# Optimization experiments

Measured on AMD Instinct MI355X. Metric: run time of the kernel, lower is better.

The kernel has to match this reference:

```python
import jax, jax.numpy as jnp
import numpy as np

B, T, D_MODEL = 4, 4096, 512
HEADS, BUCKET_SIZE, N_HASHES = 8, 64, 4
DIM_HEAD = D_MODEL // HEADS  # 64
D_FFN = 2048
N_BUCKETS = T // BUCKET_SIZE  # 64
SELF_ATTN_VALUE = -5e4  # reformer TOKEN_SELF_ATTN_VALUE


def setup_inputs() -> dict:
    key = jax.random.key(0)
    ks = jax.random.split(key, 16)
    s = 0.02
    return {
        'x': jax.random.normal(ks[0], (B, T, D_MODEL), jnp.float32),
        'rotations': jax.random.normal(ks[1], (DIM_HEAD, N_HASHES, N_BUCKETS // 2), jnp.float32),
        'w_qk': jax.random.normal(ks[2], (D_MODEL, D_MODEL), jnp.float32) * s,
        'w_v': jax.random.normal(ks[3], (D_MODEL, D_MODEL), jnp.float32) * s,
        'w_out': jax.random.normal(ks[4], (D_MODEL, D_MODEL), jnp.float32) * s,
        'b_out': jnp.zeros((D_MODEL,), jnp.float32),
        'ln1_g': jnp.ones((D_MODEL,), jnp.float32),
        'ln1_b': jnp.zeros((D_MODEL,), jnp.float32),
        'w1': jax.random.normal(ks[5], (D_FFN, D_MODEL), jnp.float32) * s,
        'b1': jnp.zeros((D_FFN,), jnp.float32),
        'w2': jax.random.normal(ks[6], (D_MODEL, D_FFN), jnp.float32) * s,
        'b2': jnp.zeros((D_MODEL,), jnp.float32),
        'ln2_g': jnp.ones((D_MODEL,), jnp.float32),
        'ln2_b': jnp.zeros((D_MODEL,), jnp.float32),
    }


def layer_norm(x, g, b, eps=1e-6):
    m = x.mean(-1, keepdims=True)
    v = ((x - m) ** 2).mean(-1, keepdims=True)
    return (x - m) / jnp.sqrt(v + eps) * g + b


def look_one_back(x):
    # concat each chunk with the previous chunk (wrap-around), along in-chunk axis
    prev = jnp.roll(x, 1, axis=1)
    return jnp.concatenate([x, prev], axis=2)


def lsh_attention(qk, v, rotations):
    # qk, v: (bh, t, d) with shared-QK; rotations: (d, n_hashes, n_buckets//2)
    bh, t, d = qk.shape
    # --- hash: random rotations, argmax over [R, -R] ---
    rot = jnp.einsum('btf,fhi->bhti', qk, rotations)
    rot = jnp.concatenate([rot, -rot], axis=-1)        # (bh, H, t, n_buckets)
    buckets = jnp.argmax(rot, axis=-1)                 # (bh, H, t)
    buckets = buckets + (jnp.arange(N_HASHES) * N_BUCKETS)[None, :, None]
    buckets = buckets.reshape(bh, N_HASHES * t)
    # --- sort by (bucket, position) ---
    ticker = jnp.arange(N_HASHES * t)
    buckets_and_t = t * buckets + (ticker % t)[None, :]
    sticker = jnp.argsort(buckets_and_t, axis=-1)      # stable sort
    undo_sort = jnp.argsort(sticker, axis=-1)
    st = sticker % t                                   # original positions, sorted order
    sqk = jnp.take_along_axis(qk, st[..., None], axis=1)
    sv = jnp.take_along_axis(v, st[..., None], axis=1)
    # --- chunk: n_hashes*n_buckets chunks of bucket_size tokens ---
    n_chunks = N_HASHES * N_BUCKETS
    bq_t = st.reshape(bh, n_chunks, -1)
    bqk = sqk.reshape(bh, n_chunks, -1, d)
    bv = sv.reshape(bh, n_chunks, -1, d)
    bk = bqk / jnp.clip(jnp.linalg.norm(bqk, axis=-1, keepdims=True), 1e-6, None)
    bk = look_one_back(bk)
    bv = look_one_back(bv)
    bkv_t = look_one_back(bq_t)
    # --- local attention within chunk (+ previous chunk) ---
    dots = jnp.einsum('bcid,bcjd->bcij', bqk, bk) * (DIM_HEAD ** -0.5)
    self_mask = bq_t[..., None] == bkv_t[..., None, :]
    dots = jnp.where(self_mask, SELF_ATTN_VALUE, dots)
    logits = jax.nn.logsumexp(dots, axis=-1, keepdims=True)
    probs = jnp.exp(dots - logits)
    bo = jnp.einsum('bcij,bcjd->bcid', probs, bv)
    # --- unsort and combine hash rounds by softmax over round logits ---
    so = bo.reshape(bh, N_HASHES * t, d)
    slogits = logits.reshape(bh, N_HASHES * t)
    o = jnp.take_along_axis(so, undo_sort[..., None], axis=1).reshape(bh, N_HASHES, t, d)
    lg = jnp.take_along_axis(slogits, undo_sort, axis=1).reshape(bh, N_HASHES, t, 1)
    w = jnp.exp(lg - jax.nn.logsumexp(lg, axis=1, keepdims=True))
    return (o * w).sum(axis=1)                         # (bh, t, d)


def reference(x, rotations, w_qk, w_v, w_out, b_out, ln1_g, ln1_b, w1, b1, w2, b2, ln2_g, ln2_b):
    b, t, _ = x.shape
    qk = x @ w_qk.T
    v = x @ w_v.T

    def split_heads(u):
        return u.reshape(b, t, HEADS, DIM_HEAD).transpose(0, 2, 1, 3).reshape(b * HEADS, t, DIM_HEAD)

    attn = lsh_attention(split_heads(qk), split_heads(v), rotations)
    attn = attn.reshape(b, HEADS, t, DIM_HEAD).transpose(0, 2, 1, 3).reshape(b, t, D_MODEL)
    attn = attn @ w_out.T + b_out
    # residual + LN (dropout is identity at inference)
    h = layer_norm(attn + x, ln1_g, ln1_b)
    # position-wise FFN with its own residual + LN
    f = jax.nn.relu(h @ w1.T + b1) @ w2.T + b2
    return layer_norm(f + h, ln2_g, ln2_b)
```

## Files before the change

kernel.cpp:

```cpp
#include <hip/hip_runtime.h>
#include <stdint.h>

typedef unsigned short u16;
typedef __attribute__((ext_vector_type(4))) int   i32x4;
typedef __attribute__((ext_vector_type(4))) float f32x4;

__device__ __forceinline__ u16 f2bf(float x){
  unsigned int u = __float_as_uint(x);
  u += 0x7FFFu + ((u >> 16) & 1u);
  return (u16)(u >> 16);
}
__device__ __forceinline__ float bf2f(u16 h){
  return __uint_as_float(((unsigned int)h) << 16);
}
__device__ __forceinline__ unsigned int cvtpk_bf16(float lo, float hi){
  unsigned int r;
  asm("v_cvt_pk_bf16_f32 %0, %1, %2" : "=v"(r) : "v"(lo), "v"(hi));
  return r;
}
__device__ __forceinline__ f32x4 mfma16(i32x4 a, i32x4 b, f32x4 c){
  asm("v_mfma_f32_16x16x32_bf16 %0, %1, %2, %0" : "+v"(c) : "v"(a), "v"(b));
  return c;
}
__device__ __forceinline__ f32x4 acc_fence(f32x4 c){
  asm volatile("s_nop 7\ns_nop 7" : "+v"(c));
  return c;
}
__device__ __forceinline__ void gl_lds16(const void* g, void* l){
  unsigned long long ga = (unsigned long long)g;
  unsigned int la = (unsigned int)(unsigned long long)l;
  __builtin_amdgcn_global_load_lds((const __attribute__((address_space(1))) void*)ga,
                                   (__attribute__((address_space(3))) void*)la, 16, 0, 0);
}
__device__ __forceinline__ int xcd_swz(int f, int n){
  int chunk = n >> 3;
  return (f & 7) * chunk + (f >> 3);
}
__device__ __forceinline__ unsigned int f2mono(float v){
  unsigned int u = __float_as_uint(v);
  return u ^ ((unsigned int)((int)u >> 31) | 0x80000000u);
}
__device__ __forceinline__ float mono2f(unsigned int mu){
  unsigned int u = (mu & 0x80000000u) ? (mu ^ 0x80000000u) : ~mu;
  return __uint_as_float(u);
}
__device__ __forceinline__ unsigned long long shfl_xor_u64(unsigned long long x, int m){
  int lo = __shfl_xor((int)(unsigned int)(x & 0xFFFFFFFFull), m);
  int hi = __shfl_xor((int)(unsigned int)(x >> 32), m);
  return ((unsigned long long)(unsigned int)hi << 32) | (unsigned int)lo;
}

__global__ __launch_bounds__(256) void k_split(const float* __restrict__ in, u16* __restrict__ hi, u16* __restrict__ lo, int n4){
  int i = blockIdx.x*256 + threadIdx.x;
  if (i >= n4) return;
  float4 v = ((const float4*)in)[i];
  ushort4 h, l;
  h.x=f2bf(v.x); l.x=f2bf(v.x - bf2f(h.x));
  h.y=f2bf(v.y); l.y=f2bf(v.y - bf2f(h.y));
  h.z=f2bf(v.z); l.z=f2bf(v.z - bf2f(h.z));
  h.w=f2bf(v.w); l.w=f2bf(v.w - bf2f(h.w));
  ((ushort4*)hi)[i]=h; ((ushort4*)lo)[i]=l;
}

__global__ __launch_bounds__(256) void k_wprep(
    const float* __restrict__ w_qk, const float* __restrict__ w_v,
    const float* __restrict__ w_out, const float* __restrict__ w1,
    const float* __restrict__ w2, const float* __restrict__ rot,
    u16* __restrict__ wqkh, u16* __restrict__ wqkl,
    u16* __restrict__ wvb, u16* __restrict__ wob,
    u16* __restrict__ w1b, u16* __restrict__ w2b,
    u16* __restrict__ rothi, u16* __restrict__ rotlo)
{
  const int bid = blockIdx.x;
  if (bid >= 2816){
    int i = (bid - 2816)*256 + threadIdx.x;
    int d = i & 63, n = i >> 6;
    float v = rot[d*128 + n];
    u16 h = f2bf(v);
    rothi[i] = h; rotlo[i] = f2bf(v - bf2f(h));
    return;
  }
  const int i = bid*256 + threadIdx.x;
  if (i < 65536){
    float4 v = ((const float4*)w_qk)[i];
    ushort4 h, l;
    h.x=f2bf(v.x); l.x=f2bf(v.x - bf2f(h.x));
    h.y=f2bf(v.y); l.y=f2bf(v.y - bf2f(h.y));
    h.z=f2bf(v.z); l.z=f2bf(v.z - bf2f(h.z));
    h.w=f2bf(v.w); l.w=f2bf(v.w - bf2f(h.w));
    ((ushort4*)wqkh)[i]=h; ((ushort4*)wqkl)[i]=l;
    return;
  }
  const float* src; u16* dst; int j;
  if (i < 131072){ src = w_v;  dst = wvb; j = i - 65536; }
  else if (i < 196608){ src = w_out; dst = wob; j = i - 131072; }
  else if (i < 458752){ src = w1;   dst = w1b; j = i - 196608; }
  else { src = w2; dst = w2b; j = i - 458752; }
  float4 v = ((const float4*)src)[j];
  ushort4 o; o.x=f2bf(v.x); o.y=f2bf(v.y); o.z=f2bf(v.z); o.w=f2bf(v.w);
  ((ushort4*)dst)[j] = o;
}

template<int MODE>
__global__ __launch_bounds__(256) void k_gemm(
    const u16* __restrict__ A0, const u16* __restrict__ B0,
    const float* __restrict__ bias,
    float* __restrict__ Cf, u16* __restrict__ Cb,
    int M, int N, int K)
{
  const int tid = threadIdx.x;
  const int l = tid & 63, w = tid >> 6;
  const int lr = l & 15, lg = l >> 4;
  int flat = blockIdx.y * gridDim.x + blockIdx.x;
  flat = xcd_swz(flat, gridDim.x * gridDim.y);
  const int m0 = (flat / gridDim.x) * 128, n0 = (flat % gridDim.x) * 128;
  const int mbase = (w >> 1) * 64, nbase = (w & 1) * 64;

  __shared__ __align__(16) u16 As[128*64];
  __shared__ __align__(16) u16 Bs[128*64];

  f32x4 zero = {0.f,0.f,0.f,0.f};
  f32x4 acc[4][4];
  #pragma unroll
  for (int i=0;i<4;i++)
    #pragma unroll
    for (int j=0;j<4;j++) acc[i][j] = zero;

  const int row_s = tid >> 3;
  const int c16   = tid & 7;

  for (int k0 = 0; k0 < K; k0 += 64){
    #pragma unroll
    for (int q=0;q<4;q++){
      int ra = q*32 + row_s;
      int cs = c16 ^ (ra & 7);
      gl_lds16(A0 + (size_t)(m0 + ra)*K + k0 + cs*8, (char*)As + q*4096 + tid*16);
      gl_lds16(B0 + (size_t)(n0 + ra)*K + k0 + cs*8, (char*)Bs + q*4096 + tid*16);
    }
    __syncthreads();
    #pragma unroll
    for (int kk=0; kk<64; kk+=32){
      i32x4 af[4], bfr[4];
      #pragma unroll
      for (int mf=0;mf<4;mf++){
        int row = mbase + mf*16 + lr;
        af[mf] = *(const i32x4*)((const char*)As + row*128 + (((kk*2) + (lg*16)) ^ ((row&7)<<4)));
      }
      #pragma unroll
      for (int nf=0;nf<4;nf++){
        int row = nbase + nf*16 + lr;
        bfr[nf] = *(const i32x4*)((const char*)Bs + row*128 + (((kk*2) + (lg*16)) ^ ((row&7)<<4)));
      }
      #pragma unroll
      for (int mf=0;mf<4;mf++)
        #pragma unroll
        for (int nf=0;nf<4;nf++)
          acc[mf][nf] = mfma16(af[mf], bfr[nf], acc[mf][nf]);
    }
    __syncthreads();
  }

  #pragma unroll
  for (int mf=0;mf<4;mf++){
    #pragma unroll
    for (int nf=0;nf<4;nf++){
      f32x4 v = acc_fence(acc[mf][nf]);
      #pragma unroll
      for (int r=0;r<4;r++){
        int m = m0 + mbase + mf*16 + lg*4 + r;
        int n = n0 + nbase + nf*16 + lr;
        float val = v[r];
        if (MODE == 1){
          val += bias[n];
          val = fmaxf(val, 0.f);
          Cb[(size_t)m*N + n] = f2bf(val);
        } else if (MODE == 4){
          val += bias[n];
          Cb[(size_t)m*N + n] = f2bf(val);
        } else {
          int b = m >> 12, t = m & 4095, h = n >> 6, d = n & 63;
          size_t idx = ((((size_t)(b*8 + h)) << 12) + t)*64 + d;
          Cb[idx] = f2bf(val);
        }
      }
    }
  }
}

__global__ __launch_bounds__(256) void k_gemmqk(
    const u16* __restrict__ Ah, const u16* __restrict__ Al,
    const u16* __restrict__ Bh, const u16* __restrict__ Bl,
    u16* __restrict__ qb, u16* __restrict__ qlo, u16* __restrict__ kn)
{
  const int K = 512;
  const int tid = threadIdx.x;
  const int l = tid & 63, w = tid >> 6;
  const int lr = l & 15, lg = l >> 4;
  int flat = blockIdx.y * gridDim.x + blockIdx.x;
  flat = xcd_swz(flat, gridDim.x * gridDim.y);
  const int m0 = (flat >> 2) * 128, n0 = (flat & 3) * 128;
  const int mbase = (w >> 1) * 64, nbase = (w & 1) * 64;

  __shared__ __align__(16) u16 AsH[128*64];
  __shared__ __align__(16) u16 AsL[128*64];
  __shared__ __align__(16) u16 BsH[128*64];
  __shared__ __align__(16) u16 BsL[128*64];

  f32x4 zero = {0.f,0.f,0.f,0.f};
  f32x4 acc[4][4];
  #pragma unroll
  for (int i=0;i<4;i++)
    #pragma unroll
    for (int j=0;j<4;j++) acc[i][j] = zero;

  const int row_s = tid >> 3;
  const int c16   = tid & 7;

  for (int k0 = 0; k0 < K; k0 += 64){
    #pragma unroll
    for (int q=0;q<4;q++){
      int ra = q*32 + row_s;
      int cs = c16 ^ (ra & 7);
      size_t ao = (size_t)(m0 + ra)*K + k0 + cs*8;
      size_t bo = (size_t)(n0 + ra)*K + k0 + cs*8;
      gl_lds16(Ah + ao, (char*)AsH + q*4096 + tid*16);
      gl_lds16(Al + ao, (char*)AsL + q*4096 + tid*16);
      gl_lds16(Bh + bo, (char*)BsH + q*4096 + tid*16);
      gl_lds16(Bl + bo, (char*)BsL + q*4096 + tid*16);
    }
    __syncthreads();
    #pragma unroll
    for (int kk=0; kk<64; kk+=32){
      i32x4 ah[4], al[4], bh2[4], bl2[4];
      #pragma unroll
      for (int mf=0;mf<4;mf++){
        int row = mbase + mf*16 + lr;
        int off = (((kk*2) + (lg*16)) ^ ((row&7)<<4));
        ah[mf] = *(const i32x4*)((const char*)AsH + row*128 + off);
        al[mf] = *(const i32x4*)((const char*)AsL + row*128 + off);
      }
      #pragma unroll
      for (int nf=0;nf<4;nf++){
        int row = nbase + nf*16 + lr;
        int off = (((kk*2) + (lg*16)) ^ ((row&7)<<4));
        bh2[nf] = *(const i32x4*)((const char*)BsH + row*128 + off);
        bl2[nf] = *(const i32x4*)((const char*)BsL + row*128 + off);
      }
      #pragma unroll
      for (int mf=0;mf<4;mf++)
        #pragma unroll
        for (int nf=0;nf<4;nf++){
          acc[mf][nf] = mfma16(ah[mf], bh2[nf], acc[mf][nf]);
          acc[mf][nf] = mfma16(al[mf], bh2[nf], acc[mf][nf]);
          acc[mf][nf] = mfma16(ah[mf], bl2[nf], acc[mf][nf]);
        }
    }
    __syncthreads();
  }

  const int hh = (n0 + nbase) >> 6;
  #pragma unroll
  for (int mf=0;mf<4;mf++){
    f32x4 v[4];
    #pragma unroll
    for (int nf=0;nf<4;nf++) v[nf] = acc_fence(acc[mf][nf]);
    #pragma unroll
    for (int r=0;r<4;r++){
      float ss = 0.f;
      #pragma unroll
      for (int nf=0;nf<4;nf++) ss += v[nf][r]*v[nf][r];
      ss += __shfl_xor(ss, 1); ss += __shfl_xor(ss, 2);
      ss += __shfl_xor(ss, 4); ss += __shfl_xor(ss, 8);
      float scale = 0.18033688f / fmaxf(sqrtf(ss), 1e-6f);
      int m = m0 + mbase + mf*16 + lg*4 + r;
      int b = m >> 12, t = m & 4095;
      size_t rowb = ((((size_t)(b*8 + hh)) << 12) + t) * 64;
      #pragma unroll
      for (int nf=0;nf<4;nf++){
        float val = v[nf][r];
        u16 hbf = f2bf(val);
        size_t idx = rowb + nf*16 + lr;
        qb [idx] = hbf;
        qlo[idx] = f2bf(val - bf2f(hbf));
        kn [idx] = f2bf(val * scale);
      }
    }
  }
}

__global__ __launch_bounds__(256) void k_hash2(
    const u16* __restrict__ qh, const u16* __restrict__ ql,
    const u16* __restrict__ rh, const u16* __restrict__ rl,
    int* __restrict__ bkt)
{
  const int tid = threadIdx.x;
  const int l = tid & 63, w = tid >> 6, lr = l & 15, lg = l >> 4;
  __shared__ __align__(16) u16 Rh[128*64];
  __shared__ __align__(16) u16 Rl[128*64];
  {
    const int row_s = tid >> 3, c8 = tid & 7;
    #pragma unroll
    for (int q = 0; q < 4; q++){
      int ra = q*32 + row_s;
      int cs = c8 ^ (ra & 7);
      gl_lds16(rh + ra*64 + cs*8, (char*)Rh + q*4096 + tid*16);
      gl_lds16(rl + ra*64 + cs*8, (char*)Rl + q*4096 + tid*16);
    }
  }
  const int blk = xcd_swz(blockIdx.x, gridDim.x);
  const int qrow = blk*64 + w*16 + lr;
  const size_t qoff = (size_t)qrow*64;
  i32x4 qhf[2], qlf[2];
  qhf[0] = *(const i32x4*)(qh + qoff + lg*8);
  qhf[1] = *(const i32x4*)(qh + qoff + 32 + lg*8);
  qlf[0] = *(const i32x4*)(ql + qoff + lg*8);
  qlf[1] = *(const i32x4*)(ql + qoff + 32 + lg*8);
  __syncthreads();

  f32x4 zero = {0.f,0.f,0.f,0.f};
  f32x4 acc[8];
  #pragma unroll
  for (int i=0;i<8;i++) acc[i] = zero;
  #pragma unroll
  for (int ks = 0; ks < 2; ks++){
    #pragma unroll
    for (int nf = 0; nf < 8; nf++){
      int row = nf*16 + lr;
      int off = (ks*64 + lg*16) ^ ((row & 7) << 4);
      i32x4 rhf = *(const i32x4*)((const char*)Rh + row*128 + off);
      i32x4 rlf = *(const i32x4*)((const char*)Rl + row*128 + off);
      acc[nf] = mfma16(rhf, qhf[ks], acc[nf]);
      acc[nf] = mfma16(rlf, qhf[ks], acc[nf]);
      acc[nf] = mfma16(rhf, qlf[ks], acc[nf]);
    }
  }

  const int bh = qrow >> 12, t = qrow & 4095;
  #pragma unroll
  for (int hh = 0; hh < 4; hh++){
    f32x4 v0 = acc_fence(acc[2*hh]);
    f32x4 v1 = acc_fence(acc[2*hh+1]);
    unsigned long long kmax = 0, kmin = 0;
    #pragma unroll
    for (int r = 0; r < 4; r++){
      int j0 = lg*4 + r, j1 = 16 + lg*4 + r;
      unsigned int mu0 = f2mono(v0[r]), mu1 = f2mono(v1[r]);
      unsigned long long a = ((unsigned long long)mu0 << 32) | (unsigned int)(31 - j0);
      unsigned long long b = ((unsigned long long)mu1 << 32) | (unsigned int)(31 - j1);
      if (a > kmax) kmax = a;
      if (b > kmax) kmax = b;
      unsigned long long c = ((unsigned long long)(~mu0) << 32) | (unsigned int)(31 - j0);
      unsigned long long d = ((unsigned long long)(~mu1) << 32) | (unsigned int)(31 - j1);
      if (c > kmin) kmin = c;
      if (d > kmin) kmin = d;
    }
    #pragma unroll
    for (int msk = 16; msk < 64; msk <<= 1){
      unsigned long long o1 = shfl_xor_u64(kmax, msk); if (o1 > kmax) kmax = o1;
      unsigned long long o2 = shfl_xor_u64(kmin, msk); if (o2 > kmin) kmin = o2;
    }
    if (lg == 0){
      float vmax = mono2f((unsigned int)(kmax >> 32));
      int jmax = 31 - (int)(kmax & 0xFFFFFFFFull);
      float vmin = mono2f(~(unsigned int)(kmin >> 32));
      int jmin = 31 - (int)(kmin & 0xFFFFFFFFull);
      int bucket = (vmax >= -vmin) ? jmax : 32 + jmin;
      bkt[((size_t)(bh*4 + hh) << 12) + t] = bucket;
    }
  }
}

__global__ __launch_bounds__(64) void k_sort(const int* __restrict__ buckets, int* __restrict__ st){
  const int grp = blockIdx.x;
  const int t = threadIdx.x;
  __shared__ int bkL[4096];
  __shared__ int hist[64][65];
  __shared__ int tot[64];
  const size_t gbase = ((size_t)grp) << 12;
  for (int i=0;i<64;i++)
    bkL[i*64 + t] = buckets[gbase + i*64 + t];
  #pragma unroll
  for (int b=0;b<64;b++) hist[t][b] = 0;
  __syncthreads();
  for (int i=0;i<64;i++){
    int b = bkL[t*64 + i];
    hist[t][b]++;
  }
  __syncthreads();
  { int run = 0;
    for (int tt=0; tt<64; tt++){ int v = hist[tt][t]; hist[tt][t] = run; run += v; }
    tot[t] = run; }
  __syncthreads();
  { int v = tot[t]; int incl = v;
    #pragma unroll
    for (int d=1; d<64; d<<=1){ int n = __shfl_up(incl, d, 64); if (t >= d) incl += n; }
    tot[t] = incl - v; }
  __syncthreads();
  const size_t obase = (((size_t)(grp>>2)) << 14) + ((size_t)(grp&3) << 12);
  for (int i=0;i<64;i++){
    int e = t*64 + i;
    int b = bkL[e];
    int dest = tot[b] + hist[t][b];
    hist[t][b]++;
    st[obase + dest] = e;
  }
}

__global__ __launch_bounds__(256, 5) void k_attn(
    const u16* __restrict__ qb, const u16* __restrict__ kn, const u16* __restrict__ vB,
    const int* __restrict__ st, float* __restrict__ lgt_out, u16* __restrict__ bo)
{
  int flat = blockIdx.y * gridDim.x + blockIdx.x;
  flat = xcd_swz(flat, gridDim.x * gridDim.y);
  const int c = flat & 255, bh = flat >> 8;
  const int rnd = c >> 6;
  const int cprev = (c + 255) & 255;
  const int tid = threadIdx.x;
  const int l = tid & 63, w = tid >> 6, lr = l & 15, lg = l >> 4;

  __shared__ __align__(16) u16 Ks[128*64];
  __shared__ __align__(16) u16 Vt[64*128];

  const size_t stbase = ((size_t)bh) << 14;
  const size_t kvbase = ((size_t)bh) << 12;

  {
    const int rsub = l >> 3, c8 = l & 7;
    #pragma unroll
    for (int q2 = 0; q2 < 4; q2++){
      int row = w*32 + q2*8 + rsub;
      int cc = (row < 64) ? c : cprev;
      int pos = st[stbase + (cc << 6) + (row & 63)];
      int cs = c8 ^ (row & 7);
      gl_lds16(kn + (kvbase + pos)*64 + cs*8,
               (char*)Ks + (w*4 + q2)*1024 + l*16);
    }
  }

  const int pos_q16 = st[stbase + (c << 6) + (w*16 + lr)];
  i32x4 qf[2];
  #pragma unroll
  for (int ks = 0; ks < 2; ks++)
    qf[ks] = *(const i32x4*)(qb + (kvbase + pos_q16)*64 + ks*32 + lg*8);

  {
    const int pp = tid & 63, db = tid >> 6;
    const int q5 = pp & 15;
    const int K0 = (pp >> 4)*32 + 16*((q5 >> 1) & 1) + 4*(q5 >> 2) + 2*(q5 & 1);
    int cc0 = (K0 < 64) ? c : cprev;
    int p0 = st[stbase + (cc0 << 6) + (K0 & 63)];
    int p1 = st[stbase + (cc0 << 6) + ((K0 + 1) & 63)];
    const u16* r0 = vB + (kvbase + p0)*64 + db*16;
    const u16* r1 = vB + (kvbase + p1)*64 + db*16;
    uint4 a0 = *(const uint4*)r0, a1 = *(const uint4*)(r0 + 8);
    uint4 b0 = *(const uint4*)r1, b1 = *(const uint4*)(r1 + 8);
    uint av[8] = {a0.x,a0.y,a0.z,a0.w,a1.x,a1.y,a1.z,a1.w};
    uint bv[8] = {b0.x,b0.y,b0.z,b0.w,b1.x,b1.y,b1.z,b1.w};
    #pragma unroll
    for (int dd = 0; dd < 16; dd++){
      uint lo = (av[dd>>1] >> ((dd&1)*16)) & 0xFFFFu;
      uint hi = (bv[dd>>1] >> ((dd&1)*16)) & 0xFFFFu;
      int row = db*16 + dd;
      *(uint*)((char*)Vt + row*256 + ((pp*4) ^ ((row & 7) << 5))) = lo | (hi << 16);
    }
  }
  const bool bdry = (c & 63) == 0;
  int pkprev[4][4];
  if (bdry){
    #pragma unroll
    for (int nf2=0; nf2<4; nf2++)
      #pragma unroll
      for (int r=0;r<4;r++)
        pkprev[nf2][r] = st[stbase + (cprev << 6) + nf2*16 + lg*4 + r];
  }
  __syncthreads();

  f32x4 zero = {0.f,0.f,0.f,0.f};
  f32x4 s[8];
  #pragma unroll
  for (int i=0;i<8;i++) s[i] = zero;
  __builtin_amdgcn_s_setprio(1);
  #pragma unroll
  for (int ks = 0; ks < 2; ks++){
    #pragma unroll
    for (int nf = 0; nf < 8; nf++){
      int row = nf*16 + lr;
      i32x4 kf = *(const i32x4*)((const char*)Ks + row*128 + ((ks*64 + lg*16) ^ ((row&7)<<4)));
      s[nf] = mfma16(kf, qf[ks], s[nf]);
    }
  }
  __builtin_amdgcn_s_setprio(0);

  float p[8][4];
  float sum = 0.f;
  #pragma unroll
  for (int nf=0;nf<8;nf++){
    f32x4 t = acc_fence(s[nf]);
    #pragma unroll
    for (int r=0;r<4;r++){
      float e = __builtin_amdgcn_exp2f(t[r]);
      if (nf == w && (lg*4 + r) == lr) e = 0.f;
      if (nf >= 4 && bdry && pkprev[nf-4][r] == pos_q16) e = 0.f;
      p[nf][r] = e;
      sum += e;
    }
  }
  sum += __shfl_xor(sum, 16);
  sum += __shfl_xor(sum, 32);
  float lv = logf(sum);
  float inv = 1.f / sum;
  if (l < 16)
    lgt_out[((((size_t)bh) << 12) + pos_q16)*4 + rnd] = lv;

  i32x4 pa[4];
  #pragma unroll
  for (int ks=0;ks<4;ks++){
    uint w0 = cvtpk_bf16(p[2*ks][0],   p[2*ks][1]);
    uint w1 = cvtpk_bf16(p[2*ks][2],   p[2*ks][3]);
    uint w2 = cvtpk_bf16(p[2*ks+1][0], p[2*ks+1][1]);
    uint w3 = cvtpk_bf16(p[2*ks+1][2], p[2*ks+1][3]);
    i32x4 t = {(int)w0,(int)w1,(int)w2,(int)w3};
    pa[ks] = t;
  }

  f32x4 o[4];
  #pragma unroll
  for (int i=0;i<4;i++) o[i] = zero;
  __builtin_amdgcn_s_setprio(1);
  #pragma unroll
  for (int ks=0;ks<4;ks++){
    #pragma unroll
    for (int nf=0;nf<4;nf++){
      int row = nf*16 + lr;
      i32x4 vf = *(const i32x4*)((const char*)Vt + row*256 + ((ks*64 + lg*16) ^ ((row & 7) << 5)));
      o[nf] = mfma16(pa[ks], vf, o[nf]);
    }
  }
  __builtin_amdgcn_s_setprio(0);
  float invq[4]; int posq[4];
  #pragma unroll
  for (int r=0;r<4;r++){
    invq[r] = __shfl(inv, lg*4 + r, 64);
    posq[r] = __shfl(pos_q16, lg*4 + r, 64);
  }
  #pragma unroll
  for (int nf=0;nf<4;nf++){
    f32x4 ov = acc_fence(o[nf]);
    #pragma unroll
    for (int r=0;r<4;r++){
      bo[((((size_t)bh << 12) + posq[r]))*256 + rnd*64 + nf*16 + lr] = f2bf(ov[r] * invq[r]);
    }
  }
}

__global__ __launch_bounds__(256) void k_combine(const u16* __restrict__ bo, const float* __restrict__ lgt,
                                                 u16* __restrict__ attn){
  const int wid = blockIdx.x * 4 + (threadIdx.x >> 6);
  const int l = threadIdx.x & 63;
  const int bh = wid >> 12, t = wid & 4095;
  const size_t tb = (((size_t)bh) << 12) + t;
  float4 lg4 = *(const float4*)(lgt + tb*4);
  float m = fmaxf(fmaxf(lg4.x,lg4.y), fmaxf(lg4.z,lg4.w));
  float w0 = __expf(lg4.x-m), w1 = __expf(lg4.y-m), w2 = __expf(lg4.z-m), w3 = __expf(lg4.w-m);
  float inv = 1.f / (w0+w1+w2+w3);
  const u16* bp = bo + tb*256;
  float o = w0 * bf2f(bp[l]) + w1 * bf2f(bp[64+l]) + w2 * bf2f(bp[128+l]) + w3 * bf2f(bp[192+l]);
  o *= inv;
  int b = bh >> 3, h = bh & 7;
  attn[((((size_t)b) << 12) + t) * 512 + h*64 + l] = f2bf(o);
}

template<int RESF>
__global__ __launch_bounds__(256) void k_ln(const u16* __restrict__ a,
                                            const float* __restrict__ resf, const u16* __restrict__ resb,
                                            const float* __restrict__ g, const float* __restrict__ bb,
                                            float* __restrict__ of, u16* __restrict__ ob){
  const int row = blockIdx.x*4 + (threadIdx.x >> 6);
  const int l = threadIdx.x & 63;
  const size_t base = (size_t)row*512 + l*8;
  uint4 aa = *(const uint4*)(a + base);
  uint aw[4] = {aa.x, aa.y, aa.z, aa.w};
  float av[8];
  #pragma unroll
  for (int j=0;j<4;j++){
    av[2*j]   = bf2f((u16)(aw[j] & 0xFFFF));
    av[2*j+1] = bf2f((u16)(aw[j] >> 16));
  }
  float rv[8];
  if (RESF){
    float4 r0 = *(const float4*)(resf + base);
    float4 r1 = *(const float4*)(resf + base + 4);
    rv[0]=r0.x; rv[1]=r0.y; rv[2]=r0.z; rv[3]=r0.w;
    rv[4]=r1.x; rv[5]=r1.y; rv[6]=r1.z; rv[7]=r1.w;
  } else {
    uint4 rr = *(const uint4*)(resb + base);
    uint rw[4] = {rr.x, rr.y, rr.z, rr.w};
    #pragma unroll
    for (int j=0;j<4;j++){
      rv[2*j]   = bf2f((u16)(rw[j] & 0xFFFF));
      rv[2*j+1] = bf2f((u16)(rw[j] >> 16));
    }
  }
  float v[8];
  #pragma unroll
  for (int j=0;j<8;j++) v[j] = av[j] + rv[j];
  float sum = 0.f;
  #pragma unroll
  for (int j=0;j<8;j++) sum += v[j];
  #pragma unroll
  for (int msk=1; msk<64; msk<<=1) sum += __shfl_xor(sum, msk);
  float mean = sum * (1.f/512.f);
  float ss = 0.f;
  #pragma unroll
  for (int j=0;j<8;j++){ float d = v[j]-mean; ss += d*d; }
  #pragma unroll
  for (int msk=1; msk<64; msk<<=1) ss += __shfl_xor(ss, msk);
  float rstd = rsqrtf(ss * (1.f/512.f) + 1e-6f);
  float4 g0 = *(const float4*)(g + l*8),  g1 = *(const float4*)(g + l*8 + 4);
  float4 b0 = *(const float4*)(bb + l*8), b1 = *(const float4*)(bb + l*8 + 4);
  float gv[8] = {g0.x,g0.y,g0.z,g0.w,g1.x,g1.y,g1.z,g1.w};
  float bv[8] = {b0.x,b0.y,b0.z,b0.w,b1.x,b1.y,b1.z,b1.w};
  float y[8];
  #pragma unroll
  for (int j=0;j<8;j++) y[j] = (v[j]-mean)*rstd*gv[j] + bv[j];
  if (RESF){
    #pragma unroll
    for (int j=0;j<8;j++) ob[base+j] = f2bf(y[j]);
  } else {
    #pragma unroll
    for (int j=0;j<8;j++) of[base+j] = y[j];
  }
}

extern "C" void kernel_launch(void* const* d_in, const int* in_sizes, int n_in,
                              void* d_out, int out_size, void* d_ws, size_t ws_size,
                              hipStream_t stream) {
  const float* x     = (const float*)d_in[0];
  const float* rot   = (const float*)d_in[1];
  const float* w_qk  = (const float*)d_in[2];
  const float* w_v   = (const float*)d_in[3];
  const float* w_out = (const float*)d_in[4];
  const float* b_out = (const float*)d_in[5];
  const float* ln1_g = (const float*)d_in[6];
  const float* ln1_b = (const float*)d_in[7];
  const float* w1    = (const float*)d_in[8];
  const float* b1    = (const float*)d_in[9];
  const float* w2    = (const float*)d_in[10];
  const float* b2    = (const float*)d_in[11];
  const float* ln2_g = (const float*)d_in[12];
  const float* ln2_b = (const float*)d_in[13];
  float* out = (float*)d_out;

  char* p = (char*)d_ws;
  u16*   xh   = (u16*)(p);
  u16*   xl   = (u16*)(p + 16777216);
  u16*   wqkh = (u16*)(p + 33554432);
  u16*   wqkl = (u16*)(p + 34078720);
  u16*   wvb  = (u16*)(p + 34603008);
  u16*   wob  = (u16*)(p + 35127296);
  u16*   w1b  = (u16*)(p + 35651584);
  u16*   w2b  = (u16*)(p + 37748736);
  u16*   qbuf = (u16*)(p + 39845888);
  u16*   knb  = (u16*)(p + 56623104);
  u16*   vb   = (u16*)(p + 73400320);
  int*   bkt  = (int*)(p + 90177536);
  int*   stb  = (int*)(p + 92274688);
  float* lgt  = (float*)(p + 94371840);
  u16*   bo   = (u16*)(p + 96468992);
  u16*   qlo   = bo;
  u16*   rothi = (u16*)(p + 96468992 + 16777216);
  u16*   rotlo = (u16*)(p + 96468992 + 16777216 + 16384);
  u16*   attnc = xl;
  u16*   projb = qbuf;
  u16*   fb    = xl;
  u16*   hb    = xh;
  u16*   hid   = bo;

  k_split<<<8192, 256, 0, stream>>>(x, xh, xl, 16384*512/4);
  k_wprep<<<2848, 256, 0, stream>>>(w_qk, w_v, w_out, w1, w2, rot,
                                    wqkh, wqkl, wvb, wob, w1b, w2b, rothi, rotlo);
  k_gemmqk<<<dim3(4,128), 256, 0, stream>>>(xh, xl, wqkh, wqkl, qbuf, qlo, knb);
  k_gemm<3><<<dim3(4,128), 256, 0, stream>>>(xh, wvb, nullptr, nullptr, vb, 16384, 512, 512);
  k_hash2<<<2048, 256, 0, stream>>>(qbuf, qlo, rothi, rotlo, bkt);
  k_sort<<<128, 64, 0, stream>>>(bkt, stb);
  k_attn<<<dim3(256,32), 256, 0, stream>>>(qbuf, knb, vb, stb, lgt, bo);
  k_combine<<<32768, 256, 0, stream>>>(bo, lgt, attnc);
  k_gemm<4><<<dim3(4,128), 256, 0, stream>>>(attnc, wob, b_out, nullptr, projb, 16384, 512, 512);
  k_ln<1><<<4096, 256, 0, stream>>>(projb, x, nullptr, ln1_g, ln1_b, nullptr, hb);
  k_gemm<1><<<dim3(16,128), 256, 0, stream>>>(hb, w1b, b1, nullptr, hid, 16384, 2048, 512);
  k_gemm<4><<<dim3(4,128), 256, 0, stream>>>(hid, w2b, b2, nullptr, fb, 16384, 512, 2048);
  k_ln<0><<<4096, 256, 0, stream>>>(fb, nullptr, hb, ln2_g, ln2_b, out, nullptr);
}
```

Before: 282.4 us.

## Fuse QK and V projection GEMMs into one launch with smaller LDS tiles

The separate QK (split-precision) and V projection GEMM launches are merged into one 1024-block kernel whose blocks alternate between QK and V tiles. The QK path drops from a 64-wide to a 32-wide K step with a repacked swizzle so its shared memory shrinks to 32KB, and launch bounds ask for 4 blocks per CU. The aim is to remove one launch and raise occupancy so the heavier QK tiles overlap with V tiles. In exchange the QK path runs twice as many barrier iterations, and the generic GEMM loses its head-split mode 3.

New measurement: 292.3 us. 3.5% more time.

```diff
diff --git a/kernel.cpp b/kernel.cpp
--- a/kernel.cpp
+++ b/kernel.cpp
@@ -169,42 +169,32 @@
       for (int r=0;r<4;r++){
         int m = m0 + mbase + mf*16 + lg*4 + r;
         int n = n0 + nbase + nf*16 + lr;
-        float val = v[r];
-        if (MODE == 1){
-          val += bias[n];
-          val = fmaxf(val, 0.f);
-          Cb[(size_t)m*N + n] = f2bf(val);
-        } else if (MODE == 4){
-          val += bias[n];
-          Cb[(size_t)m*N + n] = f2bf(val);
-        } else {
-          int b = m >> 12, t = m & 4095, h = n >> 6, d = n & 63;
-          size_t idx = ((((size_t)(b*8 + h)) << 12) + t)*64 + d;
-          Cb[idx] = f2bf(val);
-        }
-      }
-    }
-  }
-}
-
-__global__ __launch_bounds__(256) void k_gemmqk(
+        float val = v[r] + bias[n];
+        if (MODE == 1) val = fmaxf(val, 0.f);
+        Cb[(size_t)m*N + n] = f2bf(val);
+      }
+    }
+  }
+}
+
+__global__ __launch_bounds__(256, 4) void k_gemmqkv(
     const u16* __restrict__ Ah, const u16* __restrict__ Al,
     const u16* __restrict__ Bh, const u16* __restrict__ Bl,
-    u16* __restrict__ qb, u16* __restrict__ qlo, u16* __restrict__ kn)
+    const u16* __restrict__ Bv,
+    u16* __restrict__ qb, u16* __restrict__ qlo, u16* __restrict__ kn,
+    u16* __restrict__ vb)
 {
   const int K = 512;
   const int tid = threadIdx.x;
   const int l = tid & 63, w = tid >> 6;
   const int lr = l & 15, lg = l >> 4;
-  int flat = blockIdx.y * gridDim.x + blockIdx.x;
-  flat = xcd_swz(flat, gridDim.x * gridDim.y);
-  const int m0 = (flat >> 2) * 128, n0 = (flat & 3) * 128;
+  int flat = xcd_swz(blockIdx.x, 1024);
+  const bool is_qk = (flat & 1) == 0;
+  const int id = flat >> 1;
+  const int m0 = (id >> 2) * 128, n0 = (id & 3) * 128;
   const int mbase = (w >> 1) * 64, nbase = (w & 1) * 64;
 
-  __shared__ __align__(16) u16 AsH[128*64];
-  __shared__ __align__(16) u16 AsL[128*64];
-  __shared__ __align__(16) u16 BsH[128*64];
-  __shared__ __align__(16) u16 BsL[128*64];
+  __shared__ __align__(16) char lds[32768];
 
   f32x4 zero = {0.f,0.f,0.f,0.f};
   f32x4 acc[4][4];
@@ -213,38 +203,45 @@
     #pragma unroll
     for (int j=0;j<4;j++) acc[i][j] = zero;
 
-  const int row_s = tid >> 3;
-  const int c16   = tid & 7;
-
-  for (int k0 = 0; k0 < K; k0 += 64){
-    #pragma unroll
-    for (int q=0;q<4;q++){
-      int ra = q*32 + row_s;
-      int cs = c16 ^ (ra & 7);
-      size_t ao = (size_t)(m0 + ra)*K + k0 + cs*8;
-      size_t bo = (size_t)(n0 + ra)*K + k0 + cs*8;
-      gl_lds16(Ah + ao, (char*)AsH + q*4096 + tid*16);
-      gl_lds16(Al + ao, (char*)AsL + q*4096 + tid*16);
-      gl_lds16(Bh + bo, (char*)BsH + q*4096 + tid*16);
-      gl_lds16(Bl + bo, (char*)BsL + q*4096 + tid*16);
-    }
-    __syncthreads();
-    #pragma unroll
-    for (int kk=0; kk<64; kk+=32){
+  if (is_qk){
+    char* AsH = lds;
+    char* AsL = lds + 8192;
+    char* BsH = lds + 16384;
+    char* BsL = lds + 24576;
+    const int L  = tid >> 3;
+    const int sv = (tid & 7) ^ (L & 7);
+    const int rrow = 2*L + (sv & 1);
+    const int ch   = sv >> 1;
+
+    for (int k0 = 0; k0 < K; k0 += 32){
+      #pragma unroll
+      for (int q=0;q<2;q++){
+        size_t ao = (size_t)(m0 + q*64 + rrow)*K + k0 + ch*8;
+        size_t bo2 = (size_t)(n0 + q*64 + rrow)*K + k0 + ch*8;
+        gl_lds16(Ah + ao, AsH + q*4096 + tid*16);
+        gl_lds16(Al + ao, AsL + q*4096 + tid*16);
+        gl_lds16(Bh + bo2, BsH + q*4096 + tid*16);
+        gl_lds16(Bl + bo2, BsL + q*4096 + tid*16);
+      }
+      __syncthreads();
       i32x4 ah[4], al[4], bh2[4], bl2[4];
       #pragma unroll
       for (int mf=0;mf<4;mf++){
         int row = mbase + mf*16 + lr;
-        int off = (((kk*2) + (lg*16)) ^ ((row&7)<<4));
-        ah[mf] = *(const i32x4*)((const char*)AsH + row*128 + off);
-        al[mf] = *(const i32x4*)((const char*)AsL + row*128 + off);
+        int half = row >> 6, rr = row & 63, LL = rr >> 1;
+        int ss = ((lg<<1) | (rr&1)) ^ (LL&7);
+        int off = half*4096 + LL*128 + ss*16;
+        ah[mf] = *(const i32x4*)(AsH + off);
+        al[mf] = *(const i32x4*)(AsL + off);
       }
       #pragma unroll
       for (int nf=0;nf<4;nf++){
         int row = nbase + nf*16 + lr;
-        int off = (((kk*2) + (lg*16)) ^ ((row&7)<<4));
-        bh2[nf] = *(const i32x4*)((const char*)BsH + row*128 + off);
-        bl2[nf] = *(const i32x4*)((const char*)BsL + row*128 + off);
+        int half = row >> 6, rr = row & 63, LL = rr >> 1;
+        int ss = ((lg<<1) | (rr&1)) ^ (LL&7);
+        int off = half*4096 + LL*128 + ss*16;
+        bh2[nf] = *(const i32x4*)(BsH + off);
+        bl2[nf] = *(const i32x4*)(BsL + off);
       }
       #pragma unroll
       for (int mf=0;mf<4;mf++)
@@ -254,35 +251,84 @@
           acc[mf][nf] = mfma16(al[mf], bh2[nf], acc[mf][nf]);
           acc[mf][nf] = mfma16(ah[mf], bl2[nf], acc[mf][nf]);
         }
-    }
-    __syncthreads();
-  }
-
-  const int hh = (n0 + nbase) >> 6;
-  #pragma unroll
-  for (int mf=0;mf<4;mf++){
-    f32x4 v[4];
-    #pragma unroll
-    for (int nf=0;nf<4;nf++) v[nf] = acc_fence(acc[mf][nf]);
-    #pragma unroll
-    for (int r=0;r<4;r++){
-      float ss = 0.f;
-      #pragma unroll
-      for (int nf=0;nf<4;nf++) ss += v[nf][r]*v[nf][r];
-      ss += __shfl_xor(ss, 1); ss += __shfl_xor(ss, 2);
-      ss += __shfl_xor(ss, 4); ss += __shfl_xor(ss, 8);
-      float scale = 0.18033688f / fmaxf(sqrtf(ss), 1e-6f);
-      int m = m0 + mbase + mf*16 + lg*4 + r;
-      int b = m >> 12, t = m & 4095;
-      size_t rowb = ((((size_t)(b*8 + hh)) << 12) + t) * 64;
+      __syncthreads();
+    }
+
+    const int hh = (n0 + nbase) >> 6;
+    #pragma unroll
+    for (int mf=0;mf<4;mf++){
+      f32x4 v[4];
+      #pragma unroll
+      for (int nf=0;nf<4;nf++) v[nf] = acc_fence(acc[mf][nf]);
+      #pragma unroll
+      for (int r=0;r<4;r++){
+        float ss = 0.f;
+        #pragma unroll
+        for (int nf=0;nf<4;nf++) ss += v[nf][r]*v[nf][r];
+        ss += __shfl_xor(ss, 1); ss += __shfl_xor(ss, 2);
+        ss += __shfl_xor(ss, 4); ss += __shfl_xor(ss, 8);
+        float scale = 0.18033688f / fmaxf(sqrtf(ss), 1e-6f);
+        int m = m0 + mbase + mf*16 + lg*4 + r;
+        int b = m >> 12, t = m & 4095;
+        size_t rowb = ((((size_t)(b*8 + hh)) << 12) + t) * 64;
+        #pragma unroll
+        for (int nf=0;nf<4;nf++){
+          float val = v[nf][r];
+          u16 hbf = f2bf(val);
+          size_t idx = rowb + nf*16 + lr;
+          qb [idx] = hbf;
+          qlo[idx] = f2bf(val - bf2f(hbf));
+          kn [idx] = f2bf(val * scale);
+        }
+      }
+    }
+  } else {
+    char* As = lds;
+    char* Bs = lds + 16384;
+    const int row_s = tid >> 3;
+    const int c16   = tid & 7;
+    for (int k0 = 0; k0 < K; k0 += 64){
+      #pragma unroll
+      for (int q=0;q<4;q++){
+        int ra = q*32 + row_s;
+        int cs = c16 ^ (ra & 7);
+        gl_lds16(Ah + (size_t)(m0 + ra)*K + k0 + cs*8, As + q*4096 + tid*16);
+        gl_lds16(Bv + (size_t)(n0 + ra)*K + k0 + cs*8, Bs + q*4096 + tid*16);
+      }
+      __syncthreads();
+      #pragma unroll
+      for (int kk=0; kk<64; kk+=32){
+        i32x4 af[4], bfr[4];
+        #pragma unroll
+        for (int mf=0;mf<4;mf++){
+          int row = mbase + mf*16 + lr;
+          af[mf] = *(const i32x4*)(As + row*128 + (((kk*2) + (lg*16)) ^ ((row&7)<<4)));
+        }
+        #pragma unroll
+        for (int nf=0;nf<4;nf++){
+          int row = nbase + nf*16 + lr;
+          bfr[nf] = *(const i32x4*)(Bs + row*128 + (((kk*2) + (lg*16)) ^ ((row&7)<<4)));
+        }
+        #pragma unroll
+        for (int mf=0;mf<4;mf++)
+          #pragma unroll
+          for (int nf=0;nf<4;nf++)
+            acc[mf][nf] = mfma16(af[mf], bfr[nf], acc[mf][nf]);
+      }
+      __syncthreads();
+    }
+    #pragma unroll
+    for (int mf=0;mf<4;mf++){
       #pragma unroll
       for (int nf=0;nf<4;nf++){
-        float val = v[nf][r];
-        u16 hbf = f2bf(val);
-        size_t idx = rowb + nf*16 + lr;
-        qb [idx] = hbf;
-        qlo[idx] = f2bf(val - bf2f(hbf));
-        kn [idx] = f2bf(val * scale);
+        f32x4 v = acc_fence(acc[mf][nf]);
+        #pragma unroll
+        for (int r=0;r<4;r++){
+          int m = m0 + mbase + mf*16 + lg*4 + r;
+          int n = n0 + nbase + nf*16 + lr;
+          int b = m >> 12, t = m & 4095, h = n >> 6, d = n & 63;
+          vb[((((size_t)(b*8 + h)) << 12) + t)*64 + d] = f2bf(v[r]);
+        }
       }
     }
   }
@@ -679,8 +725,7 @@
   k_split<<<8192, 256, 0, stream>>>(x, xh, xl, 16384*512/4);
   k_wprep<<<2848, 256, 0, stream>>>(w_qk, w_v, w_out, w1, w2, rot,
                                     wqkh, wqkl, wvb, wob, w1b, w2b, rothi, rotlo);
-  k_gemmqk<<<dim3(4,128), 256, 0, stream>>>(xh, xl, wqkh, wqkl, qbuf, qlo, knb);
-  k_gemm<3><<<dim3(4,128), 256, 0, stream>>>(xh, wvb, nullptr, nullptr, vb, 16384, 512, 512);
+  k_gemmqkv<<<1024, 256, 0, stream>>>(xh, xl, wqkh, wqkl, wvb, qbuf, qlo, knb, vb);
   k_hash2<<<2048, 256, 0, stream>>>(qbuf, qlo, rothi, rotlo, bkt);
   k_sort<<<128, 64, 0, stream>>>(bkt, stb);
   k_attn<<<dim3(256,32), 256, 0, stream>>>(qbuf, knb, vb, stb, lgt, bo);
```
